# Kernel tuning notes

Hardware: AMD Instinct MI355X
Metric: run time of the kernel (lower is better)

The kernel has to match this reference:

```python
import jax, jax.numpy as jnp
import numpy as np

D = 256; HD = 16; G = 16; L = 2; HOP = 2; HK = 4
N = 16384; E = 49152; B = 256
VA = 128; VB = 8
SQRT2PI = float(np.sqrt(2.0 * 3.14159))  # module uses pi=3.14159


def group_norm(x, g=G, eps=1e-5):
    # torch GroupNorm(affine=False) on [N, D, 1]: normalize over each group of D//g channels
    n, d = x.shape
    xg = x.reshape(n, g, d // g)
    m = xg.mean(-1, keepdims=True)
    v = ((xg - m) ** 2).mean(-1, keepdims=True)
    return ((xg - m) * jax.lax.rsqrt(v + eps)).reshape(n, d)


def glin(x, w):
    # grouped 1x1 conv (no bias): x [n, g*din], w [g, dout, din] -> [n, g*dout]
    g, dout, din = w.shape
    return jnp.einsum('ngd,god->ngo', x.reshape(-1, g, din), w).reshape(-1, g * dout)


def multi_embed(idx, tables):
    # OGB-style encoder: sum of per-feature embeddings. idx [M,F], tables [F,V,D]
    out = tables[0][idx[:, 0]]
    for f in range(1, tables.shape[0]):
        out = out + tables[f][idx[:, f]]
    return out


def glb(x, pre_w, pre_b, gate_w, val_w, post_w, post_b):
    # GatedLinearBlock (dropout is identity in eval)
    xx = group_norm(x @ pre_w.T + pre_b)
    xx = jax.nn.relu(glin(xx, gate_w)) * glin(xx, val_w)
    return xx @ post_w.T + post_b


def glb2(xg, xv, gate_w, val_w, post_w, post_b):
    # GatedLinearBlock2: separate gate/value inputs, GroupNorm first
    gg = jax.nn.relu(glin(group_norm(xg), gate_w))
    vv = glin(group_norm(xv), val_w)
    return (gg * vv) @ post_w.T + post_b


def forward_impl(x_feat, edge_index, edge_attr, batch, batch_size,
                 edge_distance, atom_emb, bond2d_emb, gauss_means, gauss_stds,
                 attn_w, attn_b, scale_both,
                 conv_bond_emb, conv_pre_w, conv_gate_w, conv_val_w, conv_post_w, conv_post_b, conv_scale,
                 virt_pre_w, virt_pre_b, virt_gate_w, virt_val_w, virt_post_w, virt_post_b, virt_scale,
                 att_pre_w, att_pre_b, att_q_w, att_k_w, att_v_w, att_post_w, att_post_b, att_scale,
                 main_pre_w, main_pre_b, main_gate_w, main_val_w, main_post_w, main_post_b):
    src, dst = edge_index[0], edge_index[1]
    n = x_feat.shape[0]
    deg = jnp.clip(jax.ops.segment_sum(jnp.ones_like(dst), dst, num_segments=n) - 1, 0, 3)
    # --- edge features, mode='both': fuse 2D bond embedding with 3D gaussian features ---
    h2d = multi_embed(edge_attr, bond2d_emb)                      # [E, D]
    std = jnp.abs(gauss_stds) + 0.01
    diff = (edge_distance[:, None] - gauss_means[None, :]) / std
    h3d = jnp.exp(-0.5 * diff * diff) / (SQRT2PI * std)          # [E, D]
    w = jax.nn.sigmoid(jnp.concatenate([h2d, h3d], axis=-1) @ attn_w + attn_b[0])[:, None]
    h_e = w * h2d + (1.0 - w) * h3d
    h_in = jnp.exp(scale_both)[deg] * jax.ops.segment_sum(h_e, dst, num_segments=n)
    h_in = multi_embed(x_feat, atom_emb) + h_in                   # [N, D]
    h_virt = jnp.zeros((batch_size, D), h_in.dtype)
    h_att = jnp.zeros((batch_size, 2 * D // HD, HD, HD), h_in.dtype)
    for l in range(L):
        # --- ConvMessage: hop*kernel gated message-passing sublayers ---
        x_raw, x_out = h_in, jnp.zeros_like(h_in)
        for k in range(HK):
            if k > 0 and k % HOP == 0:
                x_raw, x_out = h_in + x_out, jnp.zeros_like(h_in)
            bond = multi_embed(edge_attr, conv_bond_emb[l, k])
            xp = x_raw @ conv_pre_w[l, k].T
            msg = glb2(xp[dst] + bond, xp[src] + bond,
                       conv_gate_w[l, k], conv_val_w[l, k], conv_post_w[l, k], conv_post_b[l, k])
            x_raw = jax.ops.segment_sum(msg, dst, num_segments=n)
            x_out = x_out + jnp.exp(conv_scale[l, k])[deg] * x_raw
        h_out = h_in + x_out
        # --- VirtMessage: graph-level virtual node with residual state ---
        h_virt = jax.ops.segment_sum(h_in, batch, num_segments=batch_size) + h_virt
        h_out = h_out + (jnp.exp(virt_scale[l]) * glb(h_virt, virt_pre_w[l], virt_pre_b[l],
                          virt_gate_w[l], virt_val_w[l], virt_post_w[l], virt_post_b[l]))[batch]
        # --- AttMessage: linear attention with per-graph scatter normalization ---
        xv0 = group_norm(h_in @ att_pre_w[l].T + att_pre_b[l])
        xq = jnp.exp(glin(xv0, att_q_w[l]) / np.sqrt(HD)).reshape(n, -1, HD)   # [N,32,16]
        xk = jnp.exp(glin(xv0, att_k_w[l]) / np.sqrt(HD)).reshape(n, -1, HD)
        xv = glin(xv0, att_v_w[l]).reshape(n, -1, HD)
        xkv = jnp.einsum('bnh,bnv->bnhv', xk, xv)                               # [N,32,16,16]
        h_att = jax.ops.segment_sum(xkv, batch, num_segments=batch_size) + h_att
        xk_sum = jax.ops.segment_sum(xk, batch, num_segments=batch_size)[batch]
        xq = xq / jnp.einsum('bnh,bnh->bn', xq, xk_sum)[:, :, None]
        att_out = jnp.einsum('bnh,bnhv->bnv', xq, h_att[batch]).reshape(n, 2 * D)
        h_out = h_out + jnp.exp(att_scale[l]) * (att_out @ att_post_w[l].T + att_post_b[l])
        # --- main gated block ---
        h_in = glb(h_out, main_pre_w[l], main_pre_b[l],
                   main_gate_w[l], main_val_w[l], main_post_w[l], main_post_b[l])
    return h_in


def setup_inputs() -> dict:
    key = jax.random.key(0)
    ks = iter(jax.random.split(key, 80))
    def rn(shape, s=0.05):
        return jax.random.normal(next(ks), shape, dtype=jnp.float32) * s
    inp = {}
    inp['x_feat'] = jax.random.randint(next(ks), (N, 9), 0, VA)
    inp['edge_index'] = jax.random.randint(next(ks), (2, E), 0, N)
    inp['edge_attr'] = jax.random.randint(next(ks), (E, 3), 0, VB)
    inp['batch'] = jnp.sort(jax.random.randint(next(ks), (N,), 0, B))
    inp['batch_size'] = B
    inp['edge_distance'] = jax.random.uniform(next(ks), (E,), dtype=jnp.float32) * 4.0
    inp['atom_emb'] = rn((9, VA, D))
    inp['bond2d_emb'] = rn((3, VB, D))
    inp['gauss_means'] = jax.random.uniform(next(ks), (D,), minval=2.0, maxval=3.0)
    inp['gauss_stds'] = jax.random.uniform(next(ks), (D,), minval=1.0, maxval=1.5)
    inp['attn_w'] = rn((2 * D,))
    inp['attn_b'] = rn((1,))
    inp['scale_both'] = jnp.full((4, D), np.log(0.1), jnp.float32)
    inp['conv_bond_emb'] = rn((L, HK, 3, VB, D))
    inp['conv_pre_w'] = rn((L, HK, D, D))
    inp['conv_gate_w'] = rn((L, HK, G, HD, HD))
    inp['conv_val_w'] = rn((L, HK, G, HD, HD))
    inp['conv_post_w'] = rn((L, HK, D, D))
    inp['conv_post_b'] = rn((L, HK, D))
    inp['conv_scale'] = jnp.full((L, HK, 4, D), np.log(0.1), jnp.float32)
    inp['virt_pre_w'] = rn((L, D, D)); inp['virt_pre_b'] = rn((L, D))
    inp['virt_gate_w'] = rn((L, G, 2 * HD, HD)); inp['virt_val_w'] = rn((L, G, 2 * HD, HD))
    inp['virt_post_w'] = rn((L, D, 2 * D)); inp['virt_post_b'] = rn((L, D))
    inp['virt_scale'] = jnp.full((L, D), np.log(0.01), jnp.float32)
    inp['att_pre_w'] = rn((L, D, D)); inp['att_pre_b'] = rn((L, D))
    inp['att_q_w'] = rn((L, G, 2 * HD, HD)); inp['att_k_w'] = rn((L, G, 2 * HD, HD)); inp['att_v_w'] = rn((L, G, 2 * HD, HD))
    inp['att_post_w'] = rn((L, D, 2 * D)); inp['att_post_b'] = rn((L, D))
    inp['att_scale'] = jnp.full((L, D), np.log(0.01), jnp.float32)
    inp['main_pre_w'] = rn((L, D, D)); inp['main_pre_b'] = rn((L, D))
    inp['main_gate_w'] = rn((L, G, 3 * HD, HD)); inp['main_val_w'] = rn((L, G, 3 * HD, HD))
    inp['main_post_w'] = rn((L, D, 3 * D)); inp['main_post_b'] = rn((L, D))
    return inp


def reference(x_feat, edge_index, edge_attr, batch, batch_size, edge_distance,
              atom_emb, bond2d_emb, gauss_means, gauss_stds, attn_w, attn_b, scale_both,
              conv_bond_emb, conv_pre_w, conv_gate_w, conv_val_w, conv_post_w, conv_post_b, conv_scale,
              virt_pre_w, virt_pre_b, virt_gate_w, virt_val_w, virt_post_w, virt_post_b, virt_scale,
              att_pre_w, att_pre_b, att_q_w, att_k_w, att_v_w, att_post_w, att_post_b, att_scale,
              main_pre_w, main_pre_b, main_gate_w, main_val_w, main_post_w, main_post_b):
    return forward_impl(x_feat, edge_index, edge_attr, batch, batch_size,
                        edge_distance, atom_emb, bond2d_emb, gauss_means, gauss_stds,
                        attn_w, attn_b, scale_both,
                        conv_bond_emb, conv_pre_w, conv_gate_w, conv_val_w, conv_post_w, conv_post_b, conv_scale,
                        virt_pre_w, virt_pre_b, virt_gate_w, virt_val_w, virt_post_w, virt_post_b, virt_scale,
                        att_pre_w, att_pre_b, att_q_w, att_k_w, att_v_w, att_post_w, att_post_b, att_scale,
                        main_pre_w, main_pre_b, main_gate_w, main_val_w, main_post_w, main_post_b)
```

## Files before the change

### kernel.cpp

```cpp
#include <hip/hip_runtime.h>
#include <cstdint>
#include <cstddef>
#include <type_traits>

#define NN 16384
#define EE 49152
#define BB 256

typedef _Float16 f16;
typedef _Float16 half8 __attribute__((ext_vector_type(8)));
typedef _Float16 half4v __attribute__((ext_vector_type(4)));
typedef _Float16 half2v __attribute__((ext_vector_type(2)));
typedef float floatx4 __attribute__((ext_vector_type(4)));

#if defined(__has_builtin)
#if __has_builtin(__builtin_amdgcn_fdot2)
#define HAVE_FDOT2 1
#endif
#endif

static constexpr size_t ND = (size_t)NN * 256;


__global__ __launch_bounds__(256) void count_deg_kernel(const int* __restrict__ dst, int* __restrict__ cnt, int e) {
  int i = blockIdx.x * 256 + threadIdx.x;
  if (i < e) atomicAdd(&cnt[dst[i]], 1);
}
__global__ __launch_bounds__(256) void clip_deg_kernel(const int* __restrict__ cnt, int* __restrict__ deg, int n) {
  int i = blockIdx.x * 256 + threadIdx.x;
  if (i < n) { int v = cnt[i] - 1; deg[i] = v < 0 ? 0 : (v > 3 ? 3 : v); }
}
__global__ __launch_bounds__(256) void goff_kernel(const int* __restrict__ batch, int* __restrict__ goff, int n, int b) {
  int i = blockIdx.x * 256 + threadIdx.x;
  if (i > n) return;
  int cur = (i < n) ? batch[i] : b;
  int prev = (i == 0) ? -1 : batch[i - 1];
  for (int x = prev + 1; x <= cur; x++) goff[x] = i;
}
__global__ __launch_bounds__(256) void scan_off_kernel(const int* __restrict__ cnt, int* __restrict__ off) {
  __shared__ int part[256];
  int tid = threadIdx.x;
  int base = tid * 64;
  int s = 0;
  for (int i = 0; i < 64; i++) s += cnt[base + i];
  part[tid] = s;
  __syncthreads();
  for (int o = 1; o < 256; o <<= 1) {
    int t = (tid >= o) ? part[tid - o] : 0;
    __syncthreads();
    part[tid] += t;
    __syncthreads();
  }
  int run = (tid == 0) ? 0 : part[tid - 1];
  for (int i = 0; i < 64; i++) {
    off[base + i] = run;
    run += cnt[base + i];
  }
  if (tid == 255) off[NN] = run;
}
__global__ __launch_bounds__(256) void copy_i_kernel(const int* __restrict__ a, int* __restrict__ b, int n) {
  int i = blockIdx.x * 256 + threadIdx.x;
  if (i < n) b[i] = a[i];
}
__global__ __launch_bounds__(256) void fill_elist_kernel(const int* __restrict__ dst,
    int* __restrict__ cursor, int* __restrict__ elist, int e) {
  int i = blockIdx.x * 256 + threadIdx.x;
  if (i < e) {
    int p = atomicAdd(&cursor[dst[i]], 1);
    elist[p] = i;
  }
}
__global__ __launch_bounds__(256) void gather_edges_kernel(const int* __restrict__ elist,
    const int* __restrict__ eattr, const int* __restrict__ src, const int* __restrict__ dst,
    const float* __restrict__ edist, int* __restrict__ ea_s, int* __restrict__ src_s,
    int* __restrict__ dst_s, float* __restrict__ ed_s) {
  int j = blockIdx.x * 256 + threadIdx.x;
  if (j >= EE) return;
  int e = elist[j];
  ea_s[j * 3 + 0] = eattr[e * 3 + 0];
  ea_s[j * 3 + 1] = eattr[e * 3 + 1];
  ea_s[j * 3 + 2] = eattr[e * 3 + 2];
  src_s[j] = src[e];
  dst_s[j] = dst[e];
  ed_s[j] = edist[e];
}
__global__ __launch_bounds__(256) void add3_kernel(float* __restrict__ dst,
    const float* __restrict__ a, const float* __restrict__ b, int n4) {
  int i = blockIdx.x * 256 + threadIdx.x;
  if (i >= n4) return;
  float4 x = reinterpret_cast<const float4*>(a)[i];
  float4 y = reinterpret_cast<const float4*>(b)[i];
  x.x += y.x; x.y += y.y; x.z += y.z; x.w += y.w;
  reinterpret_cast<float4*>(dst)[i] = x;
}
__global__ __launch_bounds__(256) void add3_both_kernel(float* __restrict__ dst, f16* __restrict__ dstH,
    const float* __restrict__ a, const float* __restrict__ b, int n4) {
  int i = blockIdx.x * 256 + threadIdx.x;
  if (i >= n4) return;
  float4 x = reinterpret_cast<const float4*>(a)[i];
  float4 y = reinterpret_cast<const float4*>(b)[i];
  x.x += y.x; x.y += y.y; x.z += y.z; x.w += y.w;
  reinterpret_cast<float4*>(dst)[i] = x;
  half4v h;
  h[0] = (f16)x.x; h[1] = (f16)x.y; h[2] = (f16)x.z; h[3] = (f16)x.w;
  reinterpret_cast<half4v*>(dstH)[i] = h;
}
__global__ __launch_bounds__(256) void bcast_add_kernel(float* __restrict__ ho,
    const float* __restrict__ vo, const float* __restrict__ vs, const int* __restrict__ batch) {
  int i4 = blockIdx.x * 256 + threadIdx.x;
  int i = i4 * 4;
  int n = i >> 8, c = i & 255;
  float4 h = reinterpret_cast<const float4*>(&ho[i])[0];
  float4 v = *reinterpret_cast<const float4*>(&vo[(size_t)batch[n] * 256 + c]);
  float4 s = *reinterpret_cast<const float4*>(&vs[c]);
  h.x += expf(s.x) * v.x; h.y += expf(s.y) * v.y;
  h.z += expf(s.z) * v.z; h.w += expf(s.w) * v.w;
  *reinterpret_cast<float4*>(&ho[i]) = h;
}
__global__ __launch_bounds__(256) void f2h_kernel(const float* __restrict__ in, f16* __restrict__ out, int n4) {
  int i = blockIdx.x * 256 + threadIdx.x;
  if (i >= n4) return;
  float4 v = reinterpret_cast<const float4*>(in)[i];
  half4v o;
  o[0] = (f16)v.x; o[1] = (f16)v.y; o[2] = (f16)v.z; o[3] = (f16)v.w;
  reinterpret_cast<half4v*>(out)[i] = o;
}

template <typename OUT>
__global__ __launch_bounds__(256) void seg_reduce_kernel(const f16* __restrict__ msg,
    const int* __restrict__ off, OUT* __restrict__ out) {
  int idx = blockIdx.x * 256 + threadIdx.x;
  int n = idx >> 6, c0 = (idx & 63) * 4;
  int j0 = off[n], j1 = off[n + 1];
  float a0 = 0.f, a1 = 0.f, a2 = 0.f, a3 = 0.f;
  int j = j0;
  for (; j + 1 < j1; j += 2) {
    half4v m0 = *reinterpret_cast<const half4v*>(&msg[(size_t)j * 256 + c0]);
    half4v m1 = *reinterpret_cast<const half4v*>(&msg[(size_t)(j + 1) * 256 + c0]);
    a0 += (float)m0[0] + (float)m1[0];
    a1 += (float)m0[1] + (float)m1[1];
    a2 += (float)m0[2] + (float)m1[2];
    a3 += (float)m0[3] + (float)m1[3];
  }
  if (j < j1) {
    half4v m0 = *reinterpret_cast<const half4v*>(&msg[(size_t)j * 256 + c0]);
    a0 += (float)m0[0]; a1 += (float)m0[1]; a2 += (float)m0[2]; a3 += (float)m0[3];
  }
  if constexpr (std::is_same<OUT, float>::value) {
    float4 o = {a0, a1, a2, a3};
    *reinterpret_cast<float4*>(&out[(size_t)n * 256 + c0]) = o;
  } else {
    half4v o;
    o[0] = (f16)a0; o[1] = (f16)a1; o[2] = (f16)a2; o[3] = (f16)a3;
    *reinterpret_cast<half4v*>(&out[(size_t)n * 256 + c0]) = o;
  }
}


__global__ __launch_bounds__(256) void edge_feat_kernel(
    const int* __restrict__ ea_s, const float* __restrict__ ed_s,
    const float* __restrict__ bond2d, const float* __restrict__ gmeans,
    const float* __restrict__ gstds, const float* __restrict__ attn_w,
    const float* __restrict__ attn_b, f16* __restrict__ msg) {
  int lane = threadIdx.x & 63;
  int j = blockIdx.x * 4 + (threadIdx.x >> 6);
  if (j >= EE) return;
  int a0 = ea_s[j * 3 + 0], a1 = ea_s[j * 3 + 1], a2 = ea_s[j * 3 + 2];
  float dist = ed_s[j];
  const float SQ2PI = sqrtf(2.0f * 3.14159f);
  int c0 = lane * 4;
  float4 b0 = *reinterpret_cast<const float4*>(&bond2d[a0 * 256 + c0]);
  float4 b1 = *reinterpret_cast<const float4*>(&bond2d[2048 + a1 * 256 + c0]);
  float4 b2 = *reinterpret_cast<const float4*>(&bond2d[4096 + a2 * 256 + c0]);
  float4 gm = *reinterpret_cast<const float4*>(&gmeans[c0]);
  float4 gs = *reinterpret_cast<const float4*>(&gstds[c0]);
  float4 w2 = *reinterpret_cast<const float4*>(&attn_w[c0]);
  float4 w3 = *reinterpret_cast<const float4*>(&attn_w[256 + c0]);
  float h2[4], h3[4];
  float part = 0.f;
#pragma unroll
  for (int i = 0; i < 4; i++) {
    h2[i] = (&b0.x)[i] + (&b1.x)[i] + (&b2.x)[i];
    float sd = fabsf((&gs.x)[i]) + 0.01f;
    float df = (dist - (&gm.x)[i]) / sd;
    h3[i] = expf(-0.5f * df * df) / (SQ2PI * sd);
    part += (&w2.x)[i] * h2[i] + (&w3.x)[i] * h3[i];
  }
#pragma unroll
  for (int off = 32; off > 0; off >>= 1) part += __shfl_xor(part, off);
  float wg = 1.f / (1.f + expf(-(part + attn_b[0])));
  half4v o;
#pragma unroll
  for (int i = 0; i < 4; i++) o[i] = (f16)(wg * h2[i] + (1.f - wg) * h3[i]);
  *reinterpret_cast<half4v*>(&msg[(size_t)j * 256 + c0]) = o;
}

__global__ __launch_bounds__(256) void atom_finish_kernel(
    const int* __restrict__ xf, const float* __restrict__ emb,
    const float* __restrict__ scale_both, const int* __restrict__ deg,
    const float* __restrict__ tmp, float* __restrict__ h_in, f16* __restrict__ h_inH) {
  int idx = blockIdx.x * 256 + threadIdx.x;
  int n = idx >> 6, c = (idx & 63) * 4;
  float a0 = 0.f, a1 = 0.f, a2 = 0.f, a3 = 0.f;
#pragma unroll
  for (int f = 0; f < 9; f++) {
    int v = xf[n * 9 + f];
    float4 e = *reinterpret_cast<const float4*>(&emb[((size_t)(f * 128 + v)) * 256 + c]);
    a0 += e.x; a1 += e.y; a2 += e.z; a3 += e.w;
  }
  int dg = deg[n];
  float4 s = *reinterpret_cast<const float4*>(&scale_both[dg * 256 + c]);
  float4 t = *reinterpret_cast<const float4*>(&tmp[(size_t)n * 256 + c]);
  float4 r;
  r.x = a0 + expf(s.x) * t.x; r.y = a1 + expf(s.y) * t.y;
  r.z = a2 + expf(s.z) * t.z; r.w = a3 + expf(s.w) * t.w;
  *reinterpret_cast<float4*>(&h_in[(size_t)n * 256 + c]) = r;
  half4v h;
  h[0] = (f16)r.x; h[1] = (f16)r.y; h[2] = (f16)r.z; h[3] = (f16)r.w;
  *reinterpret_cast<half4v*>(&h_inH[(size_t)n * 256 + c]) = h;
}

template <int MODE>
__global__ __launch_bounds__(256) void hgemm_kernel(
    const f16* __restrict__ A, const f16* __restrict__ W,
    const float* __restrict__ bias, const float* __restrict__ scale,
    const int* __restrict__ cnt, const int* __restrict__ deg,
    float* __restrict__ C, float* __restrict__ Cadd, f16* __restrict__ Cf, int K) {
  __shared__ f16 Ah[128 * 40];
  __shared__ f16 Wh[64 * 40];
  const int tid = threadIdx.x;
  const int row0 = blockIdx.x * 128, col0 = blockIdx.y * 64;
  const int lane = tid & 63;
  const int wave = tid >> 6;
  const int wr = (wave >> 1) * 64, wc = (wave & 1) * 32;
  const floatx4 fz = {0.f, 0.f, 0.f, 0.f};
  floatx4 acc[4][2];
#pragma unroll
  for (int m = 0; m < 4; m++)
#pragma unroll
    for (int n = 0; n < 2; n++) acc[m][n] = fz;
  const int q0 = tid * 2;
  const int rA0 = q0 >> 2, pA0 = q0 & 3;
  const int rA1 = (q0 + 1) >> 2, pA1 = (q0 + 1) & 3;
  const int rW = tid >> 2, pW = tid & 3;
  const int kb = (lane >> 4) * 8;
  const int fr = lane & 15;
  uint4 a0 = *reinterpret_cast<const uint4*>(&A[(size_t)(row0 + rA0) * K + pA0 * 8]);
  uint4 a1 = *reinterpret_cast<const uint4*>(&A[(size_t)(row0 + rA1) * K + pA1 * 8]);
  uint4 w0 = *reinterpret_cast<const uint4*>(&W[(size_t)(col0 + rW) * K + pW * 8]);
  for (int k0 = 0;;) {
    *reinterpret_cast<uint4*>(&Ah[rA0 * 40 + pA0 * 8]) = a0;
    *reinterpret_cast<uint4*>(&Ah[rA1 * 40 + pA1 * 8]) = a1;
    *reinterpret_cast<uint4*>(&Wh[rW * 40 + pW * 8]) = w0;
    __syncthreads();
    int kn = k0 + 32;
    if (kn < K) {
      a0 = *reinterpret_cast<const uint4*>(&A[(size_t)(row0 + rA0) * K + kn + pA0 * 8]);
      a1 = *reinterpret_cast<const uint4*>(&A[(size_t)(row0 + rA1) * K + kn + pA1 * 8]);
      w0 = *reinterpret_cast<const uint4*>(&W[(size_t)(col0 + rW) * K + kn + pW * 8]);
    }
    half8 af[4], wf[2];
#pragma unroll
    for (int m = 0; m < 4; m++)
      af[m] = *reinterpret_cast<const half8*>(&Ah[(wr + m * 16 + fr) * 40 + kb]);
#pragma unroll
    for (int n = 0; n < 2; n++)
      wf[n] = *reinterpret_cast<const half8*>(&Wh[(wc + n * 16 + fr) * 40 + kb]);
#pragma unroll
    for (int m = 0; m < 4; m++)
#pragma unroll
      for (int n = 0; n < 2; n++)
        acc[m][n] = __builtin_amdgcn_mfma_f32_16x16x32_f16(af[m], wf[n], acc[m][n], 0, 0, 0);
    if (kn >= K) break;
    __syncthreads();
    k0 = kn;
  }
  const int rl4 = (lane >> 4) * 4, cl = lane & 15;
#pragma unroll
  for (int m = 0; m < 4; m++) {
#pragma unroll
    for (int i = 0; i < 4; i++) {
      int row = row0 + wr + m * 16 + rl4 + i;
      float cb = (MODE >= 4) ? (float)cnt[row] : 1.f;
      int dg = (MODE >= 4) ? deg[row] : 0;
#pragma unroll
      for (int n = 0; n < 2; n++) {
        int col = col0 + wc + n * 16 + cl;
        float v = acc[m][n][i];
        size_t oi = (size_t)row * 256 + col;
        if (MODE >= 4) {
          v += cb * bias[col];
          float sc = expf(scale[dg * 256 + col]);
          if (MODE == 4) Cadd[oi] += sc * v;
          else Cadd[oi] = sc * v;
          if (Cf) Cf[oi] = (f16)v;
        } else if (MODE == 2) {
          v += bias[col];
          float nv = Cadd[oi] + expf(scale[col]) * v;
          if (C) C[oi] = nv;
          if (Cf) Cf[oi] = (f16)nv;
        } else {
          if (bias) v += bias[col];
          if (C) C[oi] = v;
          if (Cf) Cf[oi] = (f16)v;
        }
      }
    }
  }
}

__global__ __launch_bounds__(256) void conv_edge_kernel(
    const f16* __restrict__ xp, const int* __restrict__ ea_s,
    const int* __restrict__ src_s, const int* __restrict__ dst_s,
    const float* __restrict__ bond_emb, const float* __restrict__ gate_w,
    const float* __restrict__ val_w, f16* __restrict__ msg) {
  __shared__ float sg[16 * 260];
  __shared__ float sv[16 * 260];
  int tid = threadIdx.x;
  for (int i = tid; i < 4096; i += 256) {
    int g = i >> 8, rem = i & 255;
    sg[g * 260 + rem] = gate_w[i];
    sv[g * 260 + rem] = val_w[i];
  }
  __syncthreads();
  int idx = blockIdx.x * 256 + tid;
  int j = idx >> 4, g = idx & 15;
  int a0 = ea_s[j * 3 + 0], a1 = ea_s[j * 3 + 1], a2 = ea_s[j * 3 + 2];
  int d = dst_s[j], s = src_s[j];
  half8 xd0 = *reinterpret_cast<const half8*>(&xp[(size_t)d * 256 + g * 16]);
  half8 xd1 = *reinterpret_cast<const half8*>(&xp[(size_t)d * 256 + g * 16 + 8]);
  half8 xs0 = *reinterpret_cast<const half8*>(&xp[(size_t)s * 256 + g * 16]);
  half8 xs1 = *reinterpret_cast<const half8*>(&xp[(size_t)s * 256 + g * 16 + 8]);
  const float4* b0p = reinterpret_cast<const float4*>(&bond_emb[a0 * 256 + g * 16]);
  const float4* b1p = reinterpret_cast<const float4*>(&bond_emb[2048 + a1 * 256 + g * 16]);
  const float4* b2p = reinterpret_cast<const float4*>(&bond_emb[4096 + a2 * 256 + g * 16]);
  float xg[16], xv[16];
  float mg = 0.f, mv = 0.f;
#pragma unroll
  for (int q = 0; q < 4; q++) {
    float4 b0 = b0p[q], b1 = b1p[q], b2 = b2p[q];
#pragma unroll
    for (int t = 0; t < 4; t++) {
      int i = q * 4 + t;
      float bo = (&b0.x)[t] + (&b1.x)[t] + (&b2.x)[t];
      float xd = (i < 8) ? (float)xd0[i & 7] : (float)xd1[i & 7];
      float xs = (i < 8) ? (float)xs0[i & 7] : (float)xs1[i & 7];
      xg[i] = xd + bo;
      xv[i] = xs + bo;
      mg += xg[i];
      mv += xv[i];
    }
  }
  mg *= (1.f / 16.f);
  mv *= (1.f / 16.f);
  float vg = 0.f, vv = 0.f;
#pragma unroll
  for (int i = 0; i < 16; i++) {
    float dg_ = xg[i] - mg, dv_ = xv[i] - mv;
    vg += dg_ * dg_;
    vv += dv_ * dv_;
  }
  float rg = rsqrtf(vg * (1.f / 16.f) + 1e-5f);
  float rv = rsqrtf(vv * (1.f / 16.f) + 1e-5f);
#pragma unroll
  for (int i = 0; i < 16; i++) {
    xg[i] = (xg[i] - mg) * rg;
    xv[i] = (xv[i] - mv) * rv;
  }
  f16 res[16];
#pragma unroll
  for (int o = 0; o < 16; o++) {
    const float4* gp = reinterpret_cast<const float4*>(&sg[g * 260 + o * 16]);
    const float4* vp = reinterpret_cast<const float4*>(&sv[g * 260 + o * 16]);
    float ag = 0.f, av = 0.f;
#pragma unroll
    for (int q = 0; q < 4; q++) {
      float4 gq = gp[q], vq = vp[q];
#pragma unroll
      for (int t = 0; t < 4; t++) {
        ag += xg[q * 4 + t] * (&gq.x)[t];
        av += xv[q * 4 + t] * (&vq.x)[t];
      }
    }
    res[o] = (f16)(fmaxf(ag, 0.f) * av);
  }
  uint4* op = reinterpret_cast<uint4*>(&msg[(size_t)j * 256 + g * 16]);
  op[0] = reinterpret_cast<const uint4*>(res)[0];
  op[1] = reinterpret_cast<const uint4*>(res)[1];
}

template <int DOUT>
__global__ __launch_bounds__(256) void glb_mid_kernel(
    const float* __restrict__ X, const float* __restrict__ gate_w,
    const float* __restrict__ val_w, f16* __restrict__ out) {
  constexpr int RS = DOUT * 16 + 8;
  __shared__ f16 sg[16 * RS];
  __shared__ f16 sv[16 * RS];
  int tid = threadIdx.x;
  for (int i = tid; i < 16 * DOUT * 16; i += 256) {
    int g = i / (DOUT * 16), rem = i % (DOUT * 16);
    sg[g * RS + rem] = (f16)gate_w[i];
    sv[g * RS + rem] = (f16)val_w[i];
  }
  __syncthreads();
  int idx = blockIdx.x * 256 + tid;
  int n = idx >> 4, g = idx & 15;
  float x[16];
  float m = 0.f;
  const float4* xp4 = reinterpret_cast<const float4*>(&X[(size_t)n * 256 + g * 16]);
#pragma unroll
  for (int q = 0; q < 4; q++) {
    float4 xq = xp4[q];
#pragma unroll
    for (int t = 0; t < 4; t++) {
      x[q * 4 + t] = (&xq.x)[t];
      m += (&xq.x)[t];
    }
  }
  m *= (1.f / 16.f);
  float v = 0.f;
#pragma unroll
  for (int i = 0; i < 16; i++) {
    float d_ = x[i] - m;
    v += d_ * d_;
  }
  float r = rsqrtf(v * (1.f / 16.f) + 1e-5f);
#pragma unroll
  for (int i = 0; i < 16; i++) x[i] = (x[i] - m) * r;
#ifdef HAVE_FDOT2
  half2v xh[8];
#pragma unroll
  for (int q = 0; q < 8; q++) { xh[q][0] = (f16)x[2 * q]; xh[q][1] = (f16)x[2 * q + 1]; }
#endif
  const f16* gRow = &sg[g * RS];
  const f16* vRow = &sv[g * RS];
  f16 res[DOUT];
#pragma unroll
  for (int o = 0; o < DOUT; o++) {
    half8 gA = *reinterpret_cast<const half8*>(&gRow[o * 16]);
    half8 gB = *reinterpret_cast<const half8*>(&gRow[o * 16 + 8]);
    half8 vA = *reinterpret_cast<const half8*>(&vRow[o * 16]);
    half8 vB = *reinterpret_cast<const half8*>(&vRow[o * 16 + 8]);
    float ag = 0.f, av = 0.f;
#ifdef HAVE_FDOT2
#pragma unroll
    for (int q = 0; q < 4; q++) {
      half2v gq = {gA[2 * q], gA[2 * q + 1]};
      half2v g2 = {gB[2 * q], gB[2 * q + 1]};
      half2v vq = {vA[2 * q], vA[2 * q + 1]};
      half2v v2 = {vB[2 * q], vB[2 * q + 1]};
      ag = __builtin_amdgcn_fdot2(xh[q], gq, ag, false);
      ag = __builtin_amdgcn_fdot2(xh[q + 4], g2, ag, false);
      av = __builtin_amdgcn_fdot2(xh[q], vq, av, false);
      av = __builtin_amdgcn_fdot2(xh[q + 4], v2, av, false);
    }
#else
#pragma unroll
    for (int i = 0; i < 8; i++) {
      ag += x[i] * (float)gA[i] + x[i + 8] * (float)gB[i];
      av += x[i] * (float)vA[i] + x[i + 8] * (float)vB[i];
    }
#endif
    res[o] = (f16)(fmaxf(ag, 0.f) * av);
  }
  f16* op = &out[(size_t)n * (16 * DOUT) + g * DOUT];
#pragma unroll
  for (int q = 0; q < DOUT / 8; q++)
    *reinterpret_cast<half8*>(&op[q * 8]) = *reinterpret_cast<const half8*>(&res[q * 8]);
}

__global__ __launch_bounds__(256) void gn_vec_kernel(float* __restrict__ X) {
  int idx = blockIdx.x * 256 + threadIdx.x;
  int n = idx >> 6, q = idx & 63;
  float4 x = *reinterpret_cast<const float4*>(&X[(size_t)n * 256 + q * 4]);
  float s = x.x + x.y + x.z + x.w;
  float s2 = x.x * x.x + x.y * x.y + x.z * x.z + x.w * x.w;
  s += __shfl_xor(s, 1); s2 += __shfl_xor(s2, 1);
  s += __shfl_xor(s, 2); s2 += __shfl_xor(s2, 2);
  float m = s * (1.f / 16.f);
  float var = s2 * (1.f / 16.f) - m * m;
  float r = rsqrtf(var + 1e-5f);
  x.x = (x.x - m) * r; x.y = (x.y - m) * r;
  x.z = (x.z - m) * r; x.w = (x.w - m) * r;
  *reinterpret_cast<float4*>(&X[(size_t)n * 256 + q * 4]) = x;
}

__global__ __launch_bounds__(256) void att_graph_kernel(
    const float* __restrict__ xv0, const float* __restrict__ k_w,
    const float* __restrict__ v_w, const int* __restrict__ goff,
    float* __restrict__ h_att, float* __restrict__ xk_sum) {
  __shared__ float kx[8][512];
  __shared__ float vx[8][512];
  __shared__ float rows[8][256];
  const int tid = threadIdx.x, b = blockIdx.x;
  float wk0[16], wv0[16], wk1[16], wv1[16];
#pragma unroll
  for (int i = 0; i < 4; i++) {
    float4 k0 = *reinterpret_cast<const float4*>(&k_w[tid * 16 + i * 4]);
    float4 v0 = *reinterpret_cast<const float4*>(&v_w[tid * 16 + i * 4]);
    float4 k1 = *reinterpret_cast<const float4*>(&k_w[(tid + 256) * 16 + i * 4]);
    float4 v1 = *reinterpret_cast<const float4*>(&v_w[(tid + 256) * 16 + i * 4]);
    wk0[i * 4 + 0] = k0.x; wk0[i * 4 + 1] = k0.y; wk0[i * 4 + 2] = k0.z; wk0[i * 4 + 3] = k0.w;
    wv0[i * 4 + 0] = v0.x; wv0[i * 4 + 1] = v0.y; wv0[i * 4 + 2] = v0.z; wv0[i * 4 + 3] = v0.w;
    wk1[i * 4 + 0] = k1.x; wk1[i * 4 + 1] = k1.y; wk1[i * 4 + 2] = k1.z; wk1[i * 4 + 3] = k1.w;
    wv1[i * 4 + 0] = v1.x; wv1[i * 4 + 1] = v1.y; wv1[i * 4 + 2] = v1.z; wv1[i * 4 + 3] = v1.w;
  }
  float hacc[2][16];
  const float* hg = &h_att[(size_t)b * 8192];
#pragma unroll
  for (int c = 0; c < 2; c++) {
    int p = tid + c * 256;
    int head = p >> 4, h = p & 15;
#pragma unroll
    for (int j = 0; j < 16; j++) hacc[c][j] = hg[h * 512 + head * 16 + j];
  }
  float ks0 = 0.f, ks1 = 0.f;
  const int n0 = goff[b], n1 = goff[b + 1];
  const int g0 = tid >> 5, g1 = (tid + 256) >> 5;
  float r[8];
#pragma unroll
  for (int nn = 0; nn < 8; nn++) {
    int n = n0 + nn;
    r[nn] = (n < n1) ? xv0[(size_t)n * 256 + tid] : 0.f;
  }
  for (int nbase = n0; nbase < n1; nbase += 8) {
#pragma unroll
    for (int nn = 0; nn < 8; nn++) rows[nn][tid] = r[nn];
    __syncthreads();
#pragma unroll
    for (int nn = 0; nn < 8; nn++) {
      int n = nbase + 8 + nn;
      r[nn] = (n < n1) ? xv0[(size_t)n * 256 + tid] : 0.f;
    }
#pragma unroll
    for (int nn = 0; nn < 8; nn++) {
      const float4* rp0 = reinterpret_cast<const float4*>(&rows[nn][g0 * 16]);
      const float4* rp1 = reinterpret_cast<const float4*>(&rows[nn][g1 * 16]);
      float aK0 = 0.f, aV0 = 0.f, aK1 = 0.f, aV1 = 0.f;
#pragma unroll
      for (int q = 0; q < 4; q++) {
        float4 x0 = rp0[q], x1 = rp1[q];
#pragma unroll
        for (int t = 0; t < 4; t++) {
          float e0 = (&x0.x)[t], e1 = (&x1.x)[t];
          aK0 += e0 * wk0[q * 4 + t];
          aV0 += e0 * wv0[q * 4 + t];
          aK1 += e1 * wk1[q * 4 + t];
          aV1 += e1 * wv1[q * 4 + t];
        }
      }
      bool valid = (nbase + nn) < n1;
      float ek0 = valid ? expf(aK0 * 0.25f) : 0.f;
      float ek1 = valid ? expf(aK1 * 0.25f) : 0.f;
      kx[nn][tid] = ek0;
      kx[nn][tid + 256] = ek1;
      vx[nn][tid] = aV0;
      vx[nn][tid + 256] = aV1;
      ks0 += ek0;
      ks1 += ek1;
    }
    __syncthreads();
#pragma unroll
    for (int c = 0; c < 2; c++) {
      int p = tid + c * 256;
      int head = p >> 4, h = p & 15;
#pragma unroll
      for (int nn = 0; nn < 8; nn++) {
        float kk = kx[nn][head * 16 + h];
        const float4* vp = reinterpret_cast<const float4*>(&vx[nn][head * 16]);
#pragma unroll
        for (int q = 0; q < 4; q++) {
          float4 vq = vp[q];
          hacc[c][q * 4 + 0] += kk * vq.x;
          hacc[c][q * 4 + 1] += kk * vq.y;
          hacc[c][q * 4 + 2] += kk * vq.z;
          hacc[c][q * 4 + 3] += kk * vq.w;
        }
      }
    }
    __syncthreads();
  }
  float* hgo = &h_att[(size_t)b * 8192];
#pragma unroll
  for (int c = 0; c < 2; c++) {
    int p = tid + c * 256;
    int head = p >> 4, h = p & 15;
#pragma unroll
    for (int j = 0; j < 16; j++) hgo[h * 512 + head * 16 + j] = hacc[c][j];
  }
  xk_sum[(size_t)b * 512 + tid] = ks0;
  xk_sum[(size_t)b * 512 + tid + 256] = ks1;
}

__global__ __launch_bounds__(256) void att_out_kernel(
    const float* __restrict__ xv0, const float* __restrict__ q_w,
    const float* __restrict__ xk_sum, const float* __restrict__ h_att,
    const int* __restrict__ batch, f16* __restrict__ out) {
  __shared__ float sqw[16 * 260];
  int tid = threadIdx.x;
  for (int i = tid; i < 8192; i += 256) {
    int g = i >> 9, rem = i & 511;
    sqw[g * 260 + rem] = q_w[i];
  }
  __syncthreads();
  int wave = tid >> 6, lane = tid & 63;
  int n = blockIdx.x * 4 + wave;
  int head = lane >> 1, half = lane & 1;
  int g = head >> 1, j = head & 1;
  int b = batch[n];
  float x[16];
  const float4* xp4 = reinterpret_cast<const float4*>(&xv0[(size_t)n * 256 + g * 16]);
#pragma unroll
  for (int q = 0; q < 4; q++) {
    float4 xq = xp4[q];
#pragma unroll
    for (int t = 0; t < 4; t++) x[q * 4 + t] = (&xq.x)[t];
  }
  float qv[16];
  float denom = 0.f;
  const float* ks = &xk_sum[(size_t)b * 512 + head * 16];
#pragma unroll
  for (int h = 0; h < 16; h++) {
    const float4* wp = reinterpret_cast<const float4*>(&sqw[g * 260 + (j * 16 + h) * 16]);
    float a = 0.f;
#pragma unroll
    for (int q = 0; q < 4; q++) {
      float4 wq = wp[q];
#pragma unroll
      for (int t = 0; t < 4; t++) a += x[q * 4 + t] * (&wq.x)[t];
    }
    float e = expf(a * 0.25f);
    qv[h] = e;
    denom += e * ks[h];
  }
  float inv = 1.f / denom;
  float acc[8] = {0.f, 0.f, 0.f, 0.f, 0.f, 0.f, 0.f, 0.f};
  const float* hb = &h_att[(size_t)b * 8192 + head * 16 + half * 8];
#pragma unroll
  for (int h = 0; h < 16; h++) {
    float4 v0 = *reinterpret_cast<const float4*>(&hb[h * 512]);
    float4 v1 = *reinterpret_cast<const float4*>(&hb[h * 512 + 4]);
    float qh = qv[h];
    acc[0] += qh * v0.x; acc[1] += qh * v0.y; acc[2] += qh * v0.z; acc[3] += qh * v0.w;
    acc[4] += qh * v1.x; acc[5] += qh * v1.y; acc[6] += qh * v1.z; acc[7] += qh * v1.w;
  }
  half8 res;
#pragma unroll
  for (int v = 0; v < 8; v++) res[v] = (f16)(acc[v] * inv);
  *reinterpret_cast<half8*>(&out[(size_t)n * 512 + head * 16 + half * 8]) = res;
}

__global__ __launch_bounds__(256) void virt_seg_kernel(const float* __restrict__ h_in,
    const int* __restrict__ goff, float* __restrict__ h_virt) {
  int b = blockIdx.x, c = threadIdx.x;
  float acc = h_virt[(size_t)b * 256 + c];
  int n0 = goff[b], n1 = goff[b + 1];
  for (int n = n0; n < n1; n++) acc += h_in[(size_t)n * 256 + c];
  h_virt[(size_t)b * 256 + c] = acc;
}


extern "C" void kernel_launch(void* const* d_in, const int* in_sizes, int n_in,
                              void* d_out, int out_size, void* d_ws, size_t ws_size,
                              hipStream_t stream) {
  const int* x_feat = (const int*)d_in[0];
  const int* eidx = (const int*)d_in[1];
  const int* eattr = (const int*)d_in[2];
  const int* batch = (const int*)d_in[3];
  const float* edist = (const float*)d_in[5];
  const float* atom_emb = (const float*)d_in[6];
  const float* bond2d = (const float*)d_in[7];
  const float* gmeans = (const float*)d_in[8];
  const float* gstds = (const float*)d_in[9];
  const float* attn_w = (const float*)d_in[10];
  const float* attn_b = (const float*)d_in[11];
  const float* scale_both = (const float*)d_in[12];
  const float* conv_bond_emb = (const float*)d_in[13];
  const float* conv_pre_w = (const float*)d_in[14];
  const float* conv_gate_w = (const float*)d_in[15];
  const float* conv_val_w = (const float*)d_in[16];
  const float* conv_post_w = (const float*)d_in[17];
  const float* conv_post_b = (const float*)d_in[18];
  const float* conv_scale = (const float*)d_in[19];
  const float* virt_pre_w = (const float*)d_in[20];
  const float* virt_pre_b = (const float*)d_in[21];
  const float* virt_gate_w = (const float*)d_in[22];
  const float* virt_val_w = (const float*)d_in[23];
  const float* virt_post_w = (const float*)d_in[24];
  const float* virt_post_b = (const float*)d_in[25];
  const float* virt_scale = (const float*)d_in[26];
  const float* att_pre_w = (const float*)d_in[27];
  const float* att_pre_b = (const float*)d_in[28];
  const float* att_q_w = (const float*)d_in[29];
  const float* att_k_w = (const float*)d_in[30];
  const float* att_v_w = (const float*)d_in[31];
  const float* att_post_w = (const float*)d_in[32];
  const float* att_post_b = (const float*)d_in[33];
  const float* att_scale = (const float*)d_in[34];
  const float* main_pre_w = (const float*)d_in[35];
  const float* main_pre_b = (const float*)d_in[36];
  const float* main_gate_w = (const float*)d_in[37];
  const float* main_val_w = (const float*)d_in[38];
  const float* main_post_w = (const float*)d_in[39];
  const float* main_post_b = (const float*)d_in[40];

  const int* src = eidx;
  const int* dst = eidx + EE;

  float* ws = (float*)d_ws;
  float* h_in = ws;
  float* h_out = ws + ND;
  float* x_raw = ws + 2 * ND;
  float* x_out = ws + 3 * ND;
  float* nodeA = ws + 4 * ND;
  f16* h_inH = (f16*)(ws + 5 * ND);
  f16* xrawH = (f16*)(ws + 5 * ND + ND / 2);
  f16* hTmp = (f16*)(ws + 6 * ND);
  f16* msgH = (f16*)(ws + 6 * ND + ND / 2);
  float* sm = ws + 8 * ND;
  f16* hW = (f16*)sm;
  float* h_virt = sm + 1179648;
  float* h_att = h_virt + 65536;
  float* xk_sum = h_att + 2097152;
  float* vt1 = xk_sum + 131072;
  float* vout = vt1 + 65536;
  f16* vmidH = (f16*)(vout + 65536);
  f16* virtH = vmidH + 131072;
  int* cnt = (int*)(virtH + 65536);
  int* deg = cnt + NN;
  int* goff = deg + NN;
  int* off = goff + BB + 1;
  int* cursor = off + NN + 1;
  int* elist = cursor + NN;
  int* ea_s = elist + EE;
  int* src_s = ea_s + 3 * EE;
  int* dst_s = src_s + EE;
  float* ed_s = (float*)(dst_s + EE);

  f16* wCpre = hW;
  f16* wCpost = hW + 524288;
  f16* wApre = hW + 1048576;
  f16* wApost = hW + 1179648;
  f16* wMpre = hW + 1441792;
  f16* wMpost = hW + 1572864;
  f16* wVpre = hW + 1966080;
  f16* wVpost = hW + 2097152;

  auto cvt = [&](const float* in, f16* out, int n) {
    f2h_kernel<<<n / 4 / 256, 256, 0, stream>>>(in, out, n / 4);
  };

  cvt(conv_pre_w, wCpre, 524288);
  cvt(conv_post_w, wCpost, 524288);
  cvt(att_pre_w, wApre, 131072);
  cvt(att_post_w, wApost, 262144);
  cvt(main_pre_w, wMpre, 131072);
  cvt(main_post_w, wMpost, 393216);
  cvt(virt_pre_w, wVpre, 131072);
  cvt(virt_post_w, wVpost, 262144);

  (void)hipMemsetAsync(cnt, 0, NN * sizeof(int), stream);
  count_deg_kernel<<<EE / 256, 256, 0, stream>>>(dst, cnt, EE);
  clip_deg_kernel<<<NN / 256, 256, 0, stream>>>(cnt, deg, NN);
  goff_kernel<<<(NN + 256) / 256, 256, 0, stream>>>(batch, goff, NN, BB);
  scan_off_kernel<<<1, 256, 0, stream>>>(cnt, off);
  copy_i_kernel<<<NN / 256, 256, 0, stream>>>(off, cursor, NN);
  fill_elist_kernel<<<EE / 256, 256, 0, stream>>>(dst, cursor, elist, EE);
  gather_edges_kernel<<<EE / 256, 256, 0, stream>>>(elist, eattr, src, dst, edist,
                                                    ea_s, src_s, dst_s, ed_s);

  edge_feat_kernel<<<EE / 4, 256, 0, stream>>>(ea_s, ed_s, bond2d, gmeans, gstds,
                                               attn_w, attn_b, msgH);
  seg_reduce_kernel<float><<<NN / 4, 256, 0, stream>>>(msgH, off, x_out);
  atom_finish_kernel<<<NN * 64 / 256, 256, 0, stream>>>(x_feat, atom_emb, scale_both, deg,
                                                        x_out, h_in, h_inH);
  (void)hipMemsetAsync(h_virt, 0, 65536 * 4, stream);
  (void)hipMemsetAsync(h_att, 0, 2097152 * 4, stream);

  const dim3 gN(NN / 128, 4), gB(BB / 128, 4);
  const int n4 = (int)(ND / 4);

  for (int l = 0; l < 2; l++) {
    const f16* curH = h_inH;
    for (int k = 0; k < 4; k++) {
      if (k == 2) {
        add3_both_kernel<<<n4 / 256, 256, 0, stream>>>(x_raw, xrawH, h_in, x_out, n4);
        curH = xrawH;
      }
      size_t lk = (size_t)(l * 4 + k);
      hgemm_kernel<0><<<gN, 256, 0, stream>>>(curH, wCpre + lk * 65536, nullptr, nullptr,
                                              nullptr, nullptr, nullptr, nullptr, hTmp, 256);
      conv_edge_kernel<<<EE * 16 / 256, 256, 0, stream>>>(
          hTmp, ea_s, src_s, dst_s, conv_bond_emb + lk * 6144,
          conv_gate_w + lk * 4096, conv_val_w + lk * 4096, msgH);
      seg_reduce_kernel<f16><<<NN / 4, 256, 0, stream>>>(msgH, off, hTmp);
      if (k == 0 || k == 2)
        hgemm_kernel<5><<<gN, 256, 0, stream>>>(hTmp, wCpost + lk * 65536,
                                                conv_post_b + lk * 256, conv_scale + lk * 1024,
                                                cnt, deg, nullptr, x_out, xrawH, 256);
      else
        hgemm_kernel<4><<<gN, 256, 0, stream>>>(hTmp, wCpost + lk * 65536,
                                                conv_post_b + lk * 256, conv_scale + lk * 1024,
                                                cnt, deg, nullptr, x_out, xrawH, 256);
      curH = xrawH;
    }
    add3_kernel<<<n4 / 256, 256, 0, stream>>>(h_out, h_in, x_out, n4);

    virt_seg_kernel<<<BB, 256, 0, stream>>>(h_in, goff, h_virt);
    cvt(h_virt, virtH, 65536);
    hgemm_kernel<0><<<gB, 256, 0, stream>>>(virtH, wVpre + (size_t)l * 65536,
                                            virt_pre_b + (size_t)l * 256, nullptr, nullptr,
                                            nullptr, vt1, nullptr, nullptr, 256);
    glb_mid_kernel<32><<<BB * 16 / 256, 256, 0, stream>>>(
        vt1, virt_gate_w + (size_t)l * 8192, virt_val_w + (size_t)l * 8192, vmidH);
    hgemm_kernel<0><<<gB, 256, 0, stream>>>(vmidH, wVpost + (size_t)l * 131072,
                                            virt_post_b + (size_t)l * 256, nullptr, nullptr,
                                            nullptr, vout, nullptr, nullptr, 512);
    bcast_add_kernel<<<n4 / 256, 256, 0, stream>>>(
        h_out, vout, virt_scale + (size_t)l * 256, batch);

    hgemm_kernel<0><<<gN, 256, 0, stream>>>(h_inH, wApre + (size_t)l * 65536,
                                            att_pre_b + (size_t)l * 256, nullptr, nullptr,
                                            nullptr, nodeA, nullptr, nullptr, 256);
    gn_vec_kernel<<<NN * 64 / 256, 256, 0, stream>>>(nodeA);
    att_graph_kernel<<<BB, 256, 0, stream>>>(
        nodeA, att_k_w + (size_t)l * 8192, att_v_w + (size_t)l * 8192, goff, h_att, xk_sum);
    att_out_kernel<<<NN / 4, 256, 0, stream>>>(
        nodeA, att_q_w + (size_t)l * 8192, xk_sum, h_att, batch, msgH);
    hgemm_kernel<2><<<gN, 256, 0, stream>>>(msgH, wApost + (size_t)l * 131072,
                                            att_post_b + (size_t)l * 256,
                                            att_scale + (size_t)l * 256, nullptr, nullptr,
                                            nullptr, h_out, hTmp, 512);

    hgemm_kernel<0><<<gN, 256, 0, stream>>>(hTmp, wMpre + (size_t)l * 65536,
                                            main_pre_b + (size_t)l * 256, nullptr, nullptr,
                                            nullptr, nodeA, nullptr, nullptr, 256);
    glb_mid_kernel<48><<<NN * 16 / 256, 256, 0, stream>>>(
        nodeA, main_gate_w + (size_t)l * 12288, main_val_w + (size_t)l * 12288, msgH);
    float* hdst = (l == 1) ? (float*)d_out : h_in;
    f16* hdstH = (l == 1) ? nullptr : h_inH;
    hgemm_kernel<0><<<gN, 256, 0, stream>>>(msgH, wMpost + (size_t)l * 196608,
                                            main_post_b + (size_t)l * 256, nullptr, nullptr,
                                            nullptr, hdst, nullptr, hdstH, 768);
  }
}
```

Measured before the change: 1.138 ms.

## Use fp16 dot2 in conv edge kernel and split attention graph kernel across two blocks

The conv edge kernel now keeps the grouped gate/value weights in fp16 shared memory and computes the 16x16 grouped projections with packed fdot2 on fp16-converted normalized inputs. This halves shared memory traffic and the instruction count of the inner dot products, at some cost in precision. The attention graph kernel is split so each graph is handled by two blocks, one per half of the 512 key/value channels. That doubles the number of blocks to improve occupancy and halves the per-thread register arrays, but each node row is now loaded twice.

```diff
diff --git a/kernel.cpp b/kernel.cpp
--- a/kernel.cpp
+++ b/kernel.cpp
@@ -314,13 +314,14 @@
     const int* __restrict__ src_s, const int* __restrict__ dst_s,
     const float* __restrict__ bond_emb, const float* __restrict__ gate_w,
     const float* __restrict__ val_w, f16* __restrict__ msg) {
-  __shared__ float sg[16 * 260];
-  __shared__ float sv[16 * 260];
+  constexpr int RS = 264;
+  __shared__ f16 sg[16 * RS];
+  __shared__ f16 sv[16 * RS];
   int tid = threadIdx.x;
   for (int i = tid; i < 4096; i += 256) {
     int g = i >> 8, rem = i & 255;
-    sg[g * 260 + rem] = gate_w[i];
-    sv[g * 260 + rem] = val_w[i];
+    sg[g * RS + rem] = (f16)gate_w[i];
+    sv[g * RS + rem] = (f16)val_w[i];
   }
   __syncthreads();
   int idx = blockIdx.x * 256 + tid;
@@ -362,26 +363,51 @@
   }
   float rg = rsqrtf(vg * (1.f / 16.f) + 1e-5f);
   float rv = rsqrtf(vv * (1.f / 16.f) + 1e-5f);
+#ifdef HAVE_FDOT2
+  half2v xgh[8], xvh[8];
+#pragma unroll
+  for (int q = 0; q < 8; q++) {
+    xgh[q][0] = (f16)((xg[2 * q] - mg) * rg);
+    xgh[q][1] = (f16)((xg[2 * q + 1] - mg) * rg);
+    xvh[q][0] = (f16)((xv[2 * q] - mv) * rv);
+    xvh[q][1] = (f16)((xv[2 * q + 1] - mv) * rv);
+  }
+#else
 #pragma unroll
   for (int i = 0; i < 16; i++) {
     xg[i] = (xg[i] - mg) * rg;
     xv[i] = (xv[i] - mv) * rv;
   }
+#endif
+  const f16* gRow = &sg[g * RS];
+  const f16* vRow = &sv[g * RS];
   f16 res[16];
 #pragma unroll
   for (int o = 0; o < 16; o++) {
-    const float4* gp = reinterpret_cast<const float4*>(&sg[g * 260 + o * 16]);
-    const float4* vp = reinterpret_cast<const float4*>(&sv[g * 260 + o * 16]);
+    half8 gA = *reinterpret_cast<const half8*>(&gRow[o * 16]);
+    half8 gB = *reinterpret_cast<const half8*>(&gRow[o * 16 + 8]);
+    half8 vA = *reinterpret_cast<const half8*>(&vRow[o * 16]);
+    half8 vB = *reinterpret_cast<const half8*>(&vRow[o * 16 + 8]);
     float ag = 0.f, av = 0.f;
+#ifdef HAVE_FDOT2
 #pragma unroll
     for (int q = 0; q < 4; q++) {
-      float4 gq = gp[q], vq = vp[q];
-#pragma unroll
-      for (int t = 0; t < 4; t++) {
-        ag += xg[q * 4 + t] * (&gq.x)[t];
-        av += xv[q * 4 + t] * (&vq.x)[t];
-      }
-    }
+      half2v ga = {gA[2 * q], gA[2 * q + 1]};
+      half2v gb = {gB[2 * q], gB[2 * q + 1]};
+      half2v va = {vA[2 * q], vA[2 * q + 1]};
+      half2v vb = {vB[2 * q], vB[2 * q + 1]};
+      ag = __builtin_amdgcn_fdot2(xgh[q], ga, ag, false);
+      ag = __builtin_amdgcn_fdot2(xgh[q + 4], gb, ag, false);
+      av = __builtin_amdgcn_fdot2(xvh[q], va, av, false);
+      av = __builtin_amdgcn_fdot2(xvh[q + 4], vb, av, false);
+    }
+#else
+#pragma unroll
+    for (int i = 0; i < 8; i++) {
+      ag += xg[i] * (float)gA[i] + xg[i + 8] * (float)gB[i];
+      av += xv[i] * (float)vA[i] + xv[i + 8] * (float)vB[i];
+    }
+#endif
     res[o] = (f16)(fmaxf(ag, 0.f) * av);
   }
   uint4* op = reinterpret_cast<uint4*>(&msg[(size_t)j * 256 + g * 16]);
@@ -489,34 +515,29 @@
     const float* __restrict__ xv0, const float* __restrict__ k_w,
     const float* __restrict__ v_w, const int* __restrict__ goff,
     float* __restrict__ h_att, float* __restrict__ xk_sum) {
-  __shared__ float kx[8][512];
-  __shared__ float vx[8][512];
+  __shared__ float kx[8][256];
+  __shared__ float vx[8][256];
   __shared__ float rows[8][256];
-  const int tid = threadIdx.x, b = blockIdx.x;
-  float wk0[16], wv0[16], wk1[16], wv1[16];
+  const int tid = threadIdx.x;
+  const int b = blockIdx.x >> 1, half = blockIdx.x & 1;
+  const int p = half * 256 + tid;
+  const int g = p >> 5;
+  const int headLocal = tid >> 4;
+  const int head = p >> 4, h = p & 15;
+  float wk[16], wv[16];
 #pragma unroll
   for (int i = 0; i < 4; i++) {
-    float4 k0 = *reinterpret_cast<const float4*>(&k_w[tid * 16 + i * 4]);
-    float4 v0 = *reinterpret_cast<const float4*>(&v_w[tid * 16 + i * 4]);
-    float4 k1 = *reinterpret_cast<const float4*>(&k_w[(tid + 256) * 16 + i * 4]);
-    float4 v1 = *reinterpret_cast<const float4*>(&v_w[(tid + 256) * 16 + i * 4]);
-    wk0[i * 4 + 0] = k0.x; wk0[i * 4 + 1] = k0.y; wk0[i * 4 + 2] = k0.z; wk0[i * 4 + 3] = k0.w;
-    wv0[i * 4 + 0] = v0.x; wv0[i * 4 + 1] = v0.y; wv0[i * 4 + 2] = v0.z; wv0[i * 4 + 3] = v0.w;
-    wk1[i * 4 + 0] = k1.x; wk1[i * 4 + 1] = k1.y; wk1[i * 4 + 2] = k1.z; wk1[i * 4 + 3] = k1.w;
-    wv1[i * 4 + 0] = v1.x; wv1[i * 4 + 1] = v1.y; wv1[i * 4 + 2] = v1.z; wv1[i * 4 + 3] = v1.w;
-  }
-  float hacc[2][16];
+    float4 k0 = *reinterpret_cast<const float4*>(&k_w[p * 16 + i * 4]);
+    float4 v0 = *reinterpret_cast<const float4*>(&v_w[p * 16 + i * 4]);
+    wk[i * 4 + 0] = k0.x; wk[i * 4 + 1] = k0.y; wk[i * 4 + 2] = k0.z; wk[i * 4 + 3] = k0.w;
+    wv[i * 4 + 0] = v0.x; wv[i * 4 + 1] = v0.y; wv[i * 4 + 2] = v0.z; wv[i * 4 + 3] = v0.w;
+  }
+  float hacc[16];
   const float* hg = &h_att[(size_t)b * 8192];
 #pragma unroll
-  for (int c = 0; c < 2; c++) {
-    int p = tid + c * 256;
-    int head = p >> 4, h = p & 15;
-#pragma unroll
-    for (int j = 0; j < 16; j++) hacc[c][j] = hg[h * 512 + head * 16 + j];
-  }
-  float ks0 = 0.f, ks1 = 0.f;
+  for (int j = 0; j < 16; j++) hacc[j] = hg[h * 512 + head * 16 + j];
+  float ks = 0.f;
   const int n0 = goff[b], n1 = goff[b + 1];
-  const int g0 = tid >> 5, g1 = (tid + 256) >> 5;
   float r[8];
 #pragma unroll
   for (int nn = 0; nn < 8; nn++) {
@@ -534,62 +555,44 @@
     }
 #pragma unroll
     for (int nn = 0; nn < 8; nn++) {
-      const float4* rp0 = reinterpret_cast<const float4*>(&rows[nn][g0 * 16]);
-      const float4* rp1 = reinterpret_cast<const float4*>(&rows[nn][g1 * 16]);
-      float aK0 = 0.f, aV0 = 0.f, aK1 = 0.f, aV1 = 0.f;
+      const float4* rp = reinterpret_cast<const float4*>(&rows[nn][g * 16]);
+      float aK = 0.f, aV = 0.f;
 #pragma unroll
       for (int q = 0; q < 4; q++) {
-        float4 x0 = rp0[q], x1 = rp1[q];
+        float4 x0 = rp[q];
 #pragma unroll
         for (int t = 0; t < 4; t++) {
-          float e0 = (&x0.x)[t], e1 = (&x1.x)[t];
-          aK0 += e0 * wk0[q * 4 + t];
-          aV0 += e0 * wv0[q * 4 + t];
-          aK1 += e1 * wk1[q * 4 + t];
-          aV1 += e1 * wv1[q * 4 + t];
+          float e0 = (&x0.x)[t];
+          aK += e0 * wk[q * 4 + t];
+          aV += e0 * wv[q * 4 + t];
         }
       }
       bool valid = (nbase + nn) < n1;
-      float ek0 = valid ? expf(aK0 * 0.25f) : 0.f;
-      float ek1 = valid ? expf(aK1 * 0.25f) : 0.f;
-      kx[nn][tid] = ek0;
-      kx[nn][tid + 256] = ek1;
-      vx[nn][tid] = aV0;
-      vx[nn][tid + 256] = aV1;
-      ks0 += ek0;
-      ks1 += ek1;
+      float ek = valid ? expf(aK * 0.25f) : 0.f;
+      kx[nn][tid] = ek;
+      vx[nn][tid] = aV;
+      ks += ek;
     }
     __syncthreads();
 #pragma unroll
-    for (int c = 0; c < 2; c++) {
-      int p = tid + c * 256;
-      int head = p >> 4, h = p & 15;
-#pragma unroll
-      for (int nn = 0; nn < 8; nn++) {
-        float kk = kx[nn][head * 16 + h];
-        const float4* vp = reinterpret_cast<const float4*>(&vx[nn][head * 16]);
-#pragma unroll
-        for (int q = 0; q < 4; q++) {
-          float4 vq = vp[q];
-          hacc[c][q * 4 + 0] += kk * vq.x;
-          hacc[c][q * 4 + 1] += kk * vq.y;
-          hacc[c][q * 4 + 2] += kk * vq.z;
-          hacc[c][q * 4 + 3] += kk * vq.w;
-        }
+    for (int nn = 0; nn < 8; nn++) {
+      float kk = kx[nn][tid];
+      const float4* vp = reinterpret_cast<const float4*>(&vx[nn][headLocal * 16]);
+#pragma unroll
+      for (int q = 0; q < 4; q++) {
+        float4 vq = vp[q];
+        hacc[q * 4 + 0] += kk * vq.x;
+        hacc[q * 4 + 1] += kk * vq.y;
+        hacc[q * 4 + 2] += kk * vq.z;
+        hacc[q * 4 + 3] += kk * vq.w;
       }
     }
     __syncthreads();
   }
   float* hgo = &h_att[(size_t)b * 8192];
 #pragma unroll
-  for (int c = 0; c < 2; c++) {
-    int p = tid + c * 256;
-    int head = p >> 4, h = p & 15;
-#pragma unroll
-    for (int j = 0; j < 16; j++) hgo[h * 512 + head * 16 + j] = hacc[c][j];
-  }
-  xk_sum[(size_t)b * 512 + tid] = ks0;
-  xk_sum[(size_t)b * 512 + tid + 256] = ks1;
+  for (int j = 0; j < 16; j++) hgo[h * 512 + head * 16 + j] = hacc[j];
+  xk_sum[(size_t)b * 512 + p] = ks;
 }
 
 __global__ __launch_bounds__(256) void att_out_kernel(
@@ -823,7 +826,7 @@
                                             att_pre_b + (size_t)l * 256, nullptr, nullptr,
                                             nullptr, nodeA, nullptr, nullptr, 256);
     gn_vec_kernel<<<NN * 64 / 256, 256, 0, stream>>>(nodeA);
-    att_graph_kernel<<<BB, 256, 0, stream>>>(
+    att_graph_kernel<<<BB * 2, 256, 0, stream>>>(
         nodeA, att_k_w + (size_t)l * 8192, att_v_w + (size_t)l * 8192, goff, h_att, xk_sum);
     att_out_kernel<<<NN / 4, 256, 0, stream>>>(
         nodeA, att_q_w + (size_t)l * 8192, xk_sum, h_att, batch, msgH);
```

After: 1.066 ms. 1.07x faster.
